# Kernel optimization log

Measured on AMD Instinct MI355X. Metric: run time of the kernel, lower is better.

## Reference

```python
import jax, jax.numpy as jnp
import numpy as np

NUM_HEADS = 8
HEAD_DIM = 64  # hidden_dim // num_heads = 512 // 8
THRESHOLD = 0.5


def setup_inputs() -> dict:
    key = jax.random.key(0)
    ks = jax.random.split(key, 12)
    B, T, D, Hd = 4, 1024, 512, 512
    s = 0.02
    inp = {
        'x': jax.random.normal(ks[0], (B, T, D), dtype=jnp.float32),
        'Wq': jax.random.normal(ks[1], (D, Hd), dtype=jnp.float32) * s,
        'bq': jnp.zeros((Hd,), jnp.float32),
        'Wk': jax.random.normal(ks[2], (D, Hd), dtype=jnp.float32) * s,
        'bk': jnp.zeros((Hd,), jnp.float32),
        'Wv': jax.random.normal(ks[3], (D, Hd), dtype=jnp.float32) * s,
        'bv': jnp.zeros((Hd,), jnp.float32),
        'conv_w': jax.random.normal(ks[4], (NUM_HEADS,), dtype=jnp.float32) * 0.3,
        'conv_b': jnp.zeros((1,), jnp.float32),
        'Wfh': jax.random.normal(ks[5], (Hd, Hd), dtype=jnp.float32) * s,
        'bfh': jnp.zeros((Hd,), jnp.float32),
        'Wfg': jax.random.normal(ks[6], (Hd, Hd), dtype=jnp.float32) * s,
        'bfg': jnp.zeros((Hd,), jnp.float32),
        'Wrh': jax.random.normal(ks[7], (Hd, Hd), dtype=jnp.float32) * s,
        'brh': jnp.zeros((Hd,), jnp.float32),
        'Wrg': jax.random.normal(ks[8], (Hd, Hd), dtype=jnp.float32) * s,
        'brg': jnp.zeros((Hd,), jnp.float32),
    }
    return inp


def reference(x, Wq, bq, Wk, bk, Wv, bv, conv_w, conv_b,
              Wfh, bfh, Wfg, bfg, Wrh, brh, Wrg, brg):
    B, T, D = x.shape
    H, hd = NUM_HEADS, HEAD_DIM
    scale = hd ** -0.5

    q = (x @ Wq + bq).reshape(B, T, H, hd).transpose(0, 2, 1, 3)  # [B,H,T,hd]
    k = (x @ Wk + bk).reshape(B, T, H, hd).transpose(0, 2, 1, 3)
    v = (x @ Wv + bv).reshape(B, T, H, hd).transpose(0, 2, 1, 3)

    scores = jnp.einsum('bhqd,bhkd->bhqk', q, k) * scale        # [B,H,T,T]
    A_t = jax.nn.softmax(scores, axis=-1)

    # cross-head 1x1 conv: weighted sum over heads -> [B,1,T,T]
    R_f = jax.nn.sigmoid(jnp.einsum('bhqk,h->bqk', A_t, conv_w) + conv_b[0])
    R_f = R_f[:, None]                                           # [B,1,T,T]
    M_f = (R_f <= THRESHOLD).astype(A_t.dtype)
    M_r = (1.0 - R_f <= THRESHOLD).astype(A_t.dtype)

    A_f = jax.nn.softmax(A_t * M_f, axis=-1)
    A_r = jax.nn.softmax(A_t * M_r, axis=-1)

    T_f = jnp.einsum('bhqk,bhkd->bhqd', A_f, v).transpose(0, 2, 1, 3).reshape(B, T, H * hd)
    T_r = jnp.einsum('bhqk,bhkd->bhqd', A_r, v).transpose(0, 2, 1, 3).reshape(B, T, H * hd)

    F_f = T_f @ Wfh + bfh
    G_f = jax.nn.sigmoid(T_f @ Wfg + bfg)
    F_r = T_r @ Wrh + brh
    G_r = jax.nn.sigmoid(T_r @ Wrg + brg)

    G_cat = jax.nn.softmax(jnp.stack([G_f, G_r], axis=-1), axis=-1)  # [B,T,Hd,2]
    F_t = F_f * G_cat[..., 0] + F_r * G_cat[..., 1]
    return F_t
```

## Files before the change

### kernel.cpp

```cpp
#include <hip/hip_runtime.h>
#include <hip/hip_bf16.h>
#include <stdint.h>

typedef short bf16x8 __attribute__((ext_vector_type(8)));
typedef float f32x4 __attribute__((ext_vector_type(4)));

__device__ __forceinline__ unsigned short f2bf(float f) {
  union { float f; unsigned int u; } v;
  v.f = f;
  unsigned int u = v.u;
  u = (u + 0x7fffu + ((u >> 16) & 1u)) >> 16;
  return (unsigned short)u;
}

__device__ __forceinline__ unsigned int cvt_pk_bf16(float lo, float hi) {
  unsigned int r;
  asm("v_cvt_pk_bf16_f32 %0, %1, %2" : "=v"(r) : "v"(lo), "v"(hi));
  return r;
}

typedef union { bf16x8 v; unsigned int u[4]; } frag_u;

__device__ __forceinline__ void gload16(const void* g, void* lds) {
  __builtin_amdgcn_global_load_lds(
      (const __attribute__((address_space(1))) unsigned int*)(unsigned long long)g,
      (__attribute__((address_space(3))) unsigned int*)(unsigned long long)(unsigned)(unsigned long long)lds,
      16, 0, 0);
}

__device__ __forceinline__ bf16x8 lds_frag(const unsigned short* t, int row, int ch4q) {
  return *(const bf16x8*)(t + row * 64 + ((ch4q ^ (row & 7)) << 3));
}


__global__ __launch_bounds__(256) void prep_kernel(
    const float* __restrict__ x,
    const float* __restrict__ Wq, const float* __restrict__ Wk, const float* __restrict__ Wv,
    const float* __restrict__ Wfh, const float* __restrict__ Wfg,
    const float* __restrict__ Wrh, const float* __restrict__ Wrg,
    unsigned short* __restrict__ xb, unsigned short* __restrict__ wt) {
  int bid = blockIdx.x;
  int tid = threadIdx.x;
  if (bid < 256) {
    const float4* xi = (const float4*)x;
#pragma unroll
    for (int rep = 0; rep < 8; rep++) {
      int i = bid * 256 + tid + rep * 65536;
      float4 v = xi[i];
      uint2 u;
      u.x = cvt_pk_bf16(v.x, v.y);
      u.y = cvt_pk_bf16(v.z, v.w);
      *(uint2*)&xb[(size_t)i * 4] = u;
    }
  } else {
    __shared__ float tile[64][65];
    int t = bid - 256;
    int mat = t >> 6;
    t &= 63;
    int tr = (t >> 3) * 64, tc = (t & 7) * 64;
    const float* W = (mat == 0) ? Wq : (mat == 1) ? Wk : (mat == 2) ? Wv
                   : (mat == 3) ? Wfh : (mat == 4) ? Wfg : (mat == 5) ? Wrh : Wrg;
    unsigned short* Wt = wt + (size_t)mat * 512 * 512;
    for (int rep = 0; rep < 16; rep++) {
      int idx = rep * 256 + tid;
      int r = idx >> 6, c = idx & 63;
      tile[r][c] = W[(tr + r) * 512 + tc + c];
    }
    __syncthreads();
    for (int rep = 0; rep < 16; rep++) {
      int idx = rep * 256 + tid;
      int r = idx >> 6, c = idx & 63;
      Wt[(tc + r) * 512 + tr + c] = f2bf(tile[c][r]);
    }
  }
}

__global__ __launch_bounds__(256, 2) void qkv_kernel(
    const unsigned short* __restrict__ xb,
    const unsigned short* __restrict__ wtq, const unsigned short* __restrict__ wtk,
    const unsigned short* __restrict__ wtv,
    const float* __restrict__ bq, const float* __restrict__ bk, const float* __restrict__ bv,
    unsigned short* __restrict__ Qfrag, unsigned short* __restrict__ Kfrag,
    unsigned short* __restrict__ Vfrag) {
  __shared__ __attribute__((aligned(16))) unsigned short smem[32768];
  unsigned short* st0 = smem;
  unsigned short* st1 = smem + 4608;
  unsigned short* st2 = smem + 9216;
  const int m0 = blockIdx.y * 64, n0 = blockIdx.x * 64;
  const int tid = threadIdx.x, w = tid >> 6, lane = tid & 63;
  const int c = lane & 15, quad = lane >> 4;
  const int wm = w & 1, wn = w >> 1;
  const int rsel = lane >> 3, csel = lane & 7;
  const int sc = csel ^ rsel;
  const char* Ag  = (const char*)xb  + (size_t)(m0 + w * 16 + rsel) * 1024 + sc * 16;
  const char* Bgq = (const char*)wtq + (size_t)(n0 + w * 16 + rsel) * 1024 + sc * 16;
  const char* Bgk = (const char*)wtk + (size_t)(n0 + w * 16 + rsel) * 1024 + sc * 16;
  const char* Bgv = (const char*)wtv + (size_t)(n0 + w * 16 + rsel) * 1024 + sc * 16;
  const int woff = w * 1024;

  f32x4 acc[3][2][2];
  f32x4 z4 = {0.f, 0.f, 0.f, 0.f};
#pragma unroll
  for (int o = 0; o < 3; o++)
#pragma unroll
    for (int i = 0; i < 2; i++)
#pragma unroll
      for (int j = 0; j < 2; j++) acc[o][i][j] = z4;

  {
    unsigned short* base = smem;
    gload16(Ag, base + woff);              gload16(Ag + 8192, base + woff + 512);
    gload16(Bgq, base + 4096 + woff);      gload16(Bgq + 8192, base + 4096 + woff + 512);
    gload16(Bgk, base + 8192 + woff);      gload16(Bgk + 8192ull + 8192, base + 8192 + woff + 512);
    gload16(Bgv, base + 12288 + woff);     gload16(Bgv + 8192, base + 12288 + woff + 512);
  }
  __syncthreads();

  for (int ks = 0; ks < 8; ks++) {
    unsigned short* cur = smem + (ks & 1) * 16384;
    if (ks < 7) {
      unsigned short* nxt = smem + ((ks + 1) & 1) * 16384;
      const int kb = (ks + 1) * 128;
      gload16(Ag + kb, nxt + woff);          gload16(Ag + kb + 8192, nxt + woff + 512);
      gload16(Bgq + kb, nxt + 4096 + woff);  gload16(Bgq + kb + 8192, nxt + 4096 + woff + 512);
      gload16(Bgk + kb, nxt + 8192 + woff);  gload16(Bgk + kb + 8192, nxt + 8192 + woff + 512);
      gload16(Bgv + kb, nxt + 12288 + woff); gload16(Bgv + kb + 8192, nxt + 12288 + woff + 512);
    }
#pragma unroll
    for (int ch = 0; ch < 2; ch++) {
      const int cq = ch * 4 + quad;
      bf16x8 a0 = lds_frag(cur, wm * 32 + c, cq);
      bf16x8 a1 = lds_frag(cur, wm * 32 + 16 + c, cq);
#pragma unroll
      for (int nt = 0; nt < 2; nt++) {
        const int rb = wn * 32 + nt * 16 + c;
        bf16x8 fq = lds_frag(cur + 4096, rb, cq);
        bf16x8 fk = lds_frag(cur + 8192, rb, cq);
        bf16x8 fv = lds_frag(cur + 12288, rb, cq);
        acc[0][0][nt] = __builtin_amdgcn_mfma_f32_16x16x32_bf16(a0, fq, acc[0][0][nt], 0, 0, 0);
        acc[0][1][nt] = __builtin_amdgcn_mfma_f32_16x16x32_bf16(a1, fq, acc[0][1][nt], 0, 0, 0);
        acc[1][0][nt] = __builtin_amdgcn_mfma_f32_16x16x32_bf16(a0, fk, acc[1][0][nt], 0, 0, 0);
        acc[1][1][nt] = __builtin_amdgcn_mfma_f32_16x16x32_bf16(a1, fk, acc[1][1][nt], 0, 0, 0);
        acc[2][0][nt] = __builtin_amdgcn_mfma_f32_16x16x32_bf16(a0, fv, acc[2][0][nt], 0, 0, 0);
        acc[2][1][nt] = __builtin_amdgcn_mfma_f32_16x16x32_bf16(a1, fv, acc[2][1][nt], 0, 0, 0);
      }
    }
    __syncthreads();
  }

#pragma unroll
  for (int ms = 0; ms < 2; ms++)
#pragma unroll
    for (int nt = 0; nt < 2; nt++) {
      int n_l = wn * 32 + nt * 16 + c;
      int n = n0 + n_l;
      float biasq = bq[n], biask = bk[n], biasv = bv[n];
#pragma unroll
      for (int r = 0; r < 4; r++) {
        int m_l = wm * 32 + ms * 16 + quad * 4 + r;
        st0[m_l * 72 + n_l] = f2bf((acc[0][ms][nt][r] + biasq) * 0.125f);
        st1[m_l * 72 + n_l] = f2bf(acc[1][ms][nt][r] + biask);
        st2[n_l * 72 + m_l] = f2bf(acc[2][ms][nt][r] + biasv);
      }
    }
  __syncthreads();

  {
    const int h = n0 >> 6;
    const int bb = m0 >> 10, t0b = (m0 & 1023) >> 4;
#pragma unroll
    for (int sub = 0; sub < 2; sub++) {
      uint4 vq = *(uint4*)&st0[(w * 16 + c) * 72 + sub * 32 + quad * 8];
      uint4 vk = *(uint4*)&st1[(w * 16 + c) * 72 + sub * 32 + quad * 8];
      size_t base = (size_t)((bb * 64 + t0b + w) * 8192) + h * 1024 + sub * 512 + lane * 8;
      *(uint4*)&Qfrag[base] = vq;
      *(uint4*)&Kfrag[base] = vk;
    }
    const int ktq = t0b + w;
    const int ktp = ktq >> 1, half = ktq & 1;
#pragma unroll
    for (int dm = 0; dm < 4; dm++) {
      uint2 vv = *(uint2*)&st2[(dm * 16 + c) * 72 + w * 16 + quad * 4];
      size_t base = (size_t)(bb * 8 + h) * 65536 + (size_t)(ktp * 4 + dm) * 512
                  + lane * 8 + half * 4;
      *(uint2*)&Vfrag[base] = vv;
    }
  }
}

__global__ __launch_bounds__(512, 2) void attn_kernel(
    const unsigned short* __restrict__ Qfrag, const unsigned short* __restrict__ Kfrag,
    const unsigned short* __restrict__ Vfrag,
    const float* __restrict__ conv_w, const float* __restrict__ conv_b,
    unsigned short* __restrict__ Tfb, unsigned short* __restrict__ Trb) {
  const int b = blockIdx.x, qt = blockIdx.y;
  const int tid = threadIdx.x, w = tid >> 6, lane = tid & 63;
  const int c = lane & 15, quad = lane >> 4;
  __shared__ float zbuf[8][16];
  __shared__ float izbuf[8][16];
  __shared__ __attribute__((aligned(16))) float red[2 * 8 * 4 * 64 * 4];
  __shared__ float zred[2][8][16];

  f32x4 z4 = {0.f, 0.f, 0.f, 0.f};
  const float cb = conv_b[0];
  const size_t qbase = (size_t)((b * 64 + qt) * 8192) + lane * 8;
  const size_t kb0 = (size_t)((b * 64 + w * 8) * 8192) + lane * 8;
  const size_t vb0 = (size_t)(b * 8) * 65536 + lane * 8;

  f32x4 g[8];
#pragma unroll
  for (int j = 0; j < 8; j++) g[j] = {cb, cb, cb, cb};

  for (int h = 0; h < 8; h++) {
    bf16x8 qf0 = *(const bf16x8*)&Qfrag[qbase + h * 1024];
    bf16x8 qf1 = *(const bf16x8*)&Qfrag[qbase + h * 1024 + 512];
    f32x4 p[8];
    float zh = 0.f;
#pragma unroll
    for (int j = 0; j < 8; j++) {
      const size_t kb = kb0 + (size_t)j * 8192 + h * 1024;
      bf16x8 kf0 = *(const bf16x8*)&Kfrag[kb];
      bf16x8 kf1 = *(const bf16x8*)&Kfrag[kb + 512];
      f32x4 s = __builtin_amdgcn_mfma_f32_16x16x32_bf16(kf0, qf0, z4, 0, 0, 0);
      s = __builtin_amdgcn_mfma_f32_16x16x32_bf16(kf1, qf1, s, 0, 0, 0);
      p[j][0] = __expf(s[0]); p[j][1] = __expf(s[1]);
      p[j][2] = __expf(s[2]); p[j][3] = __expf(s[3]);
      zh += (p[j][0] + p[j][1]) + (p[j][2] + p[j][3]);
    }
    zh += __shfl_xor(zh, 16); zh += __shfl_xor(zh, 32);
    __syncthreads();
    if (quad == 0) zbuf[w][c] = zh;
    __syncthreads();
    float Z = ((zbuf[0][c] + zbuf[1][c]) + (zbuf[2][c] + zbuf[3][c]))
            + ((zbuf[4][c] + zbuf[5][c]) + (zbuf[6][c] + zbuf[7][c]));
    const float izq = 1.0f / Z;
    if (w == 0 && quad == 0) izbuf[h][c] = izq;
    const float cwz = conv_w[h] * izq;
#pragma unroll
    for (int j = 0; j < 8; j++) {
      g[j][0] += cwz * p[j][0]; g[j][1] += cwz * p[j][1];
      g[j][2] += cwz * p[j][2]; g[j][3] += cwz * p[j][3];
    }
  }

  unsigned int mmx[4], mmy[4];
#pragma unroll
  for (int t = 0; t < 4; t++) {
    unsigned int p0 = 0, p1 = 0;
#pragma unroll
    for (int r = 0; r < 4; r++) {
      p0 |= ((g[2 * t][r] <= 0.f ? 1u : 0u) | (g[2 * t][r] >= 0.f ? 2u : 0u)) << (8 * r);
      p1 |= ((g[2 * t + 1][r] <= 0.f ? 1u : 0u) | (g[2 * t + 1][r] >= 0.f ? 2u : 0u)) << (8 * r);
    }
    mmx[t] = p0; mmy[t] = p1;
  }
  __syncthreads();

  frag_u ones;
  ones.u[0] = 0x3F803F80u; ones.u[1] = 0x3F803F80u;
  ones.u[2] = 0x3F803F80u; ones.u[3] = 0x3F803F80u;

  const int fr = w >> 2, dmslot = w & 3;
  const size_t tbase = (size_t)(b * 1024 + qt * 16 + c) * 512;
  unsigned short* dstsel = (fr == 0) ? Tfb : Trb;

  for (int h = 0; h < 8; h++) {
    bf16x8 qf0 = *(const bf16x8*)&Qfrag[qbase + h * 1024];
    bf16x8 qf1 = *(const bf16x8*)&Qfrag[qbase + h * 1024 + 512];
    const float iz_h = izbuf[h][c];
    f32x4 accf[4], accr[4];
#pragma unroll
    for (int i = 0; i < 4; i++) { accf[i] = z4; accr[i] = z4; }
    f32x4 zf4 = z4, zr4 = z4;
#pragma unroll
    for (int t = 0; t < 4; t++) {
      const size_t kba = kb0 + (size_t)(2 * t) * 8192 + h * 1024;
      const size_t kbb = kba + 8192;
      bf16x8 ka0 = *(const bf16x8*)&Kfrag[kba];
      bf16x8 ka1 = *(const bf16x8*)&Kfrag[kba + 512];
      bf16x8 kb0f = *(const bf16x8*)&Kfrag[kbb];
      bf16x8 kb1f = *(const bf16x8*)&Kfrag[kbb + 512];
      f32x4 sa = __builtin_amdgcn_mfma_f32_16x16x32_bf16(ka0, qf0, z4, 0, 0, 0);
      sa = __builtin_amdgcn_mfma_f32_16x16x32_bf16(ka1, qf1, sa, 0, 0, 0);
      f32x4 sb = __builtin_amdgcn_mfma_f32_16x16x32_bf16(kb0f, qf0, z4, 0, 0, 0);
      sb = __builtin_amdgcn_mfma_f32_16x16x32_bf16(kb1f, qf1, sb, 0, 0, 0);
      float ea[4], eb[4];
#pragma unroll
      for (int r = 0; r < 4; r++) {
        ea[r] = __expf(__expf(sa[r]) * iz_h);
        eb[r] = __expf(__expf(sb[r]) * iz_h);
      }
      frag_u pF, pR;
      pF.u[0] = cvt_pk_bf16((mmx[t] & 0x1u)       ? ea[0] : 1.f, (mmx[t] & 0x100u)     ? ea[1] : 1.f);
      pF.u[1] = cvt_pk_bf16((mmx[t] & 0x10000u)   ? ea[2] : 1.f, (mmx[t] & 0x1000000u) ? ea[3] : 1.f);
      pF.u[2] = cvt_pk_bf16((mmy[t] & 0x1u)       ? eb[0] : 1.f, (mmy[t] & 0x100u)     ? eb[1] : 1.f);
      pF.u[3] = cvt_pk_bf16((mmy[t] & 0x10000u)   ? eb[2] : 1.f, (mmy[t] & 0x1000000u) ? eb[3] : 1.f);
      pR.u[0] = cvt_pk_bf16((mmx[t] & 0x2u)       ? ea[0] : 1.f, (mmx[t] & 0x200u)     ? ea[1] : 1.f);
      pR.u[1] = cvt_pk_bf16((mmx[t] & 0x20000u)   ? ea[2] : 1.f, (mmx[t] & 0x2000000u) ? ea[3] : 1.f);
      pR.u[2] = cvt_pk_bf16((mmy[t] & 0x2u)       ? eb[0] : 1.f, (mmy[t] & 0x200u)     ? eb[1] : 1.f);
      pR.u[3] = cvt_pk_bf16((mmy[t] & 0x20000u)   ? eb[2] : 1.f, (mmy[t] & 0x2000000u) ? eb[3] : 1.f);
      zf4 = __builtin_amdgcn_mfma_f32_16x16x32_bf16(ones.v, pF.v, zf4, 0, 0, 0);
      zr4 = __builtin_amdgcn_mfma_f32_16x16x32_bf16(ones.v, pR.v, zr4, 0, 0, 0);
      const size_t vbh = vb0 + (size_t)h * 65536 + (size_t)((w * 4 + t) * 4) * 512;
#pragma unroll
      for (int dm = 0; dm < 4; dm++) {
        bf16x8 vf = *(const bf16x8*)&Vfrag[vbh + (size_t)dm * 512];
        accf[dm] = __builtin_amdgcn_mfma_f32_16x16x32_bf16(vf, pF.v, accf[dm], 0, 0, 0);
        accr[dm] = __builtin_amdgcn_mfma_f32_16x16x32_bf16(vf, pR.v, accr[dm], 0, 0, 0);
      }
    }
    __syncthreads();
#pragma unroll
    for (int dm = 0; dm < 4; dm++) {
      *(f32x4*)&red[(((0 * 8 + w) * 4 + dm) * 64 + lane) * 4] = accf[dm];
      *(f32x4*)&red[(((1 * 8 + w) * 4 + dm) * 64 + lane) * 4] = accr[dm];
    }
    if (quad == 0) { zred[0][w][c] = zf4[0]; zred[1][w][c] = zr4[0]; }
    __syncthreads();
    {
      f32x4 o = z4;
#pragma unroll
      for (int w2 = 0; w2 < 8; w2++)
        o += *(const f32x4*)&red[(((fr * 8 + w2) * 4 + dmslot) * 64 + lane) * 4];
      float Zq = 0.f;
#pragma unroll
      for (int w2 = 0; w2 < 8; w2++) Zq += zred[fr][w2][c];
      const float iz = 1.0f / Zq;
      uint2 u;
      u.x = cvt_pk_bf16(o[0] * iz, o[1] * iz);
      u.y = cvt_pk_bf16(o[2] * iz, o[3] * iz);
      *(uint2*)&dstsel[tbase + h * 64 + dmslot * 16 + quad * 4] = u;
    }
  }
}

__global__ __launch_bounds__(256, 4) void final_kernel(
    const unsigned short* __restrict__ Tfb, const unsigned short* __restrict__ Trb,
    const unsigned short* __restrict__ wfh, const unsigned short* __restrict__ wfg,
    const unsigned short* __restrict__ wrh, const unsigned short* __restrict__ wrg,
    const float* __restrict__ bfh, const float* __restrict__ bfg,
    const float* __restrict__ brh, const float* __restrict__ brg,
    float* __restrict__ out) {
  __shared__ unsigned short Atf[32 * 64];
  __shared__ unsigned short Atr[32 * 64];
  __shared__ unsigned short Bfh[64 * 64];
  __shared__ unsigned short Bfg[64 * 64];
  __shared__ unsigned short Brh[64 * 64];
  __shared__ unsigned short Brg[64 * 64];
  const int m0 = blockIdx.y * 32, n0 = blockIdx.x * 64;
  const int tid = threadIdx.x, w = tid >> 6, lane = tid & 63;
  const int c = lane & 15, quad = lane >> 4;
  const int wm = w & 1, wn = w >> 1;
  const int rsel = lane >> 3, csel = lane & 7;
  const int sc = csel ^ rsel;
  const char* Agf = (const char*)Tfb + (size_t)(m0 + w * 8 + rsel) * 1024 + sc * 16;
  const char* Agr = (const char*)Trb + (size_t)(m0 + w * 8 + rsel) * 1024 + sc * 16;
  const char* Bg0 = (const char*)wfh + (size_t)(n0 + w * 16 + rsel) * 1024 + sc * 16;
  const char* Bg1 = (const char*)wfg + (size_t)(n0 + w * 16 + rsel) * 1024 + sc * 16;
  const char* Bg2 = (const char*)wrh + (size_t)(n0 + w * 16 + rsel) * 1024 + sc * 16;
  const char* Bg3 = (const char*)wrg + (size_t)(n0 + w * 16 + rsel) * 1024 + sc * 16;
  unsigned short* lAf = &Atf[w * 512];
  unsigned short* lAr = &Atr[w * 512];
  unsigned short* l0 = &Bfh[w * 1024];
  unsigned short* l1 = &Bfg[w * 1024];
  unsigned short* l2 = &Brh[w * 1024];
  unsigned short* l3 = &Brg[w * 1024];

  f32x4 acc[4][2];
  f32x4 z4 = {0.f, 0.f, 0.f, 0.f};
#pragma unroll
  for (int o = 0; o < 4; o++)
#pragma unroll
    for (int j = 0; j < 2; j++) acc[o][j] = z4;

  for (int ks = 0; ks < 8; ks++) {
    if (ks) __syncthreads();
    const int kb = ks * 128;
    gload16(Agf + kb, lAf);
    gload16(Agr + kb, lAr);
    gload16(Bg0 + kb, l0);   gload16(Bg0 + kb + 8192, l0 + 512);
    gload16(Bg1 + kb, l1);   gload16(Bg1 + kb + 8192, l1 + 512);
    gload16(Bg2 + kb, l2);   gload16(Bg2 + kb + 8192, l2 + 512);
    gload16(Bg3 + kb, l3);   gload16(Bg3 + kb + 8192, l3 + 512);
    __syncthreads();
#pragma unroll
    for (int ch = 0; ch < 2; ch++) {
      const int cq = ch * 4 + quad;
      bf16x8 af = lds_frag(Atf, wm * 16 + c, cq);
      bf16x8 ar = lds_frag(Atr, wm * 16 + c, cq);
#pragma unroll
      for (int nt = 0; nt < 2; nt++) {
        const int rb = wn * 32 + nt * 16 + c;
        bf16x8 f0 = lds_frag(Bfh, rb, cq);
        bf16x8 f1 = lds_frag(Bfg, rb, cq);
        bf16x8 f2 = lds_frag(Brh, rb, cq);
        bf16x8 f3 = lds_frag(Brg, rb, cq);
        acc[0][nt] = __builtin_amdgcn_mfma_f32_16x16x32_bf16(af, f0, acc[0][nt], 0, 0, 0);
        acc[1][nt] = __builtin_amdgcn_mfma_f32_16x16x32_bf16(af, f1, acc[1][nt], 0, 0, 0);
        acc[2][nt] = __builtin_amdgcn_mfma_f32_16x16x32_bf16(ar, f2, acc[2][nt], 0, 0, 0);
        acc[3][nt] = __builtin_amdgcn_mfma_f32_16x16x32_bf16(ar, f3, acc[3][nt], 0, 0, 0);
      }
    }
  }

#pragma unroll
  for (int nt = 0; nt < 2; nt++) {
    int n = n0 + wn * 32 + nt * 16 + c;
    float b0 = bfh[n], b1 = bfg[n], b2 = brh[n], b3 = brg[n];
    int t0 = m0 + wm * 16 + quad * 4;
#pragma unroll
    for (int r = 0; r < 4; r++) {
      int t = t0 + r;
      float Ff = acc[0][nt][r] + b0;
      float Gf = 1.0f / (1.0f + __expf(-(acc[1][nt][r] + b1)));
      float Fr = acc[2][nt][r] + b2;
      float Gr = 1.0f / (1.0f + __expf(-(acc[3][nt][r] + b3)));
      float ef = __expf(Gf), er = __expf(Gr);
      out[(size_t)t * 512 + n] = (Ff * ef + Fr * er) / (ef + er);
    }
  }
}

extern "C" void kernel_launch(void* const* d_in, const int* in_sizes, int n_in,
                              void* d_out, int out_size, void* d_ws, size_t ws_size,
                              hipStream_t stream) {
  const float* x   = (const float*)d_in[0];
  const float* Wq  = (const float*)d_in[1];
  const float* bq  = (const float*)d_in[2];
  const float* Wk  = (const float*)d_in[3];
  const float* bk  = (const float*)d_in[4];
  const float* Wv  = (const float*)d_in[5];
  const float* bv  = (const float*)d_in[6];
  const float* cw  = (const float*)d_in[7];
  const float* cb  = (const float*)d_in[8];
  const float* Wfh = (const float*)d_in[9];
  const float* bfh = (const float*)d_in[10];
  const float* Wfg = (const float*)d_in[11];
  const float* bfg = (const float*)d_in[12];
  const float* Wrh = (const float*)d_in[13];
  const float* brh = (const float*)d_in[14];
  const float* Wrg = (const float*)d_in[15];
  const float* brg = (const float*)d_in[16];

  char* ws = (char*)d_ws;
  const size_t MB = 1024 * 1024;
  unsigned short* xb    = (unsigned short*)(ws + 0 * MB);
  unsigned short* Qfrag = (unsigned short*)(ws + 4 * MB);
  unsigned short* Kfrag = (unsigned short*)(ws + 8 * MB);
  unsigned short* Vfrag = (unsigned short*)(ws + 12 * MB);
  unsigned short* Tfb   = (unsigned short*)(ws + 16 * MB);
  unsigned short* Trb   = (unsigned short*)(ws + 20 * MB);
  unsigned short* wt    = (unsigned short*)(ws + 24 * MB);
  const size_t WSZ = 512 * 512;

  prep_kernel<<<704, 256, 0, stream>>>(x, Wq, Wk, Wv, Wfh, Wfg, Wrh, Wrg, xb, wt);
  qkv_kernel<<<dim3(8, 64), 256, 0, stream>>>(xb, wt + 0 * WSZ, wt + 1 * WSZ, wt + 2 * WSZ,
                                              bq, bk, bv, Qfrag, Kfrag, Vfrag);
  attn_kernel<<<dim3(4, 64), 512, 0, stream>>>(Qfrag, Kfrag, Vfrag, cw, cb, Tfb, Trb);
  final_kernel<<<dim3(8, 128), 256, 0, stream>>>(Tfb, Trb, wt + 3 * WSZ, wt + 4 * WSZ,
                                                 wt + 5 * WSZ, wt + 6 * WSZ,
                                                 bfh, bfg, brh, brg, (float*)d_out);
}
```

Measured before the change: 173.5 us.

## Fix K prologue load offset, pin attn waves, enlarge final GEMM M tile

Fixes the prologue K-weight load in qkv_kernel, which read the wrong second row chunk (offset 16384 instead of 8192) and so fed wrong data into the first k-step. Replaces attn_kernel's launch_bounds min-blocks with an explicit amdgpu_waves_per_eu(2,2) register-budget hint. Doubles final_kernel's M tile from 32 to 64 rows so each weight tile loaded into LDS serves twice as many rows, halving the grid and doubling accumulators per wave. The trade-off is higher register pressure and fewer blocks in the final GEMM.

```diff
diff --git a/kernel.cpp b/kernel.cpp
--- a/kernel.cpp
+++ b/kernel.cpp
@@ -111,7 +111,7 @@
     unsigned short* base = smem;
     gload16(Ag, base + woff);              gload16(Ag + 8192, base + woff + 512);
     gload16(Bgq, base + 4096 + woff);      gload16(Bgq + 8192, base + 4096 + woff + 512);
-    gload16(Bgk, base + 8192 + woff);      gload16(Bgk + 8192ull + 8192, base + 8192 + woff + 512);
+    gload16(Bgk, base + 8192 + woff);      gload16(Bgk + 8192, base + 8192 + woff + 512);
     gload16(Bgv, base + 12288 + woff);     gload16(Bgv + 8192, base + 12288 + woff + 512);
   }
   __syncthreads();
@@ -188,7 +188,9 @@
   }
 }
 
-__global__ __launch_bounds__(512, 2) void attn_kernel(
+__global__ __launch_bounds__(512)
+__attribute__((amdgpu_waves_per_eu(2, 2)))
+void attn_kernel(
     const unsigned short* __restrict__ Qfrag, const unsigned short* __restrict__ Kfrag,
     const unsigned short* __restrict__ Vfrag,
     const float* __restrict__ conv_w, const float* __restrict__ conv_b,
@@ -334,50 +336,52 @@
   }
 }
 
-__global__ __launch_bounds__(256, 4) void final_kernel(
+__global__ __launch_bounds__(256, 2) void final_kernel(
     const unsigned short* __restrict__ Tfb, const unsigned short* __restrict__ Trb,
     const unsigned short* __restrict__ wfh, const unsigned short* __restrict__ wfg,
     const unsigned short* __restrict__ wrh, const unsigned short* __restrict__ wrg,
     const float* __restrict__ bfh, const float* __restrict__ bfg,
     const float* __restrict__ brh, const float* __restrict__ brg,
     float* __restrict__ out) {
-  __shared__ unsigned short Atf[32 * 64];
-  __shared__ unsigned short Atr[32 * 64];
+  __shared__ unsigned short Atf[64 * 64];
+  __shared__ unsigned short Atr[64 * 64];
   __shared__ unsigned short Bfh[64 * 64];
   __shared__ unsigned short Bfg[64 * 64];
   __shared__ unsigned short Brh[64 * 64];
   __shared__ unsigned short Brg[64 * 64];
-  const int m0 = blockIdx.y * 32, n0 = blockIdx.x * 64;
+  const int m0 = blockIdx.y * 64, n0 = blockIdx.x * 64;
   const int tid = threadIdx.x, w = tid >> 6, lane = tid & 63;
   const int c = lane & 15, quad = lane >> 4;
   const int wm = w & 1, wn = w >> 1;
   const int rsel = lane >> 3, csel = lane & 7;
   const int sc = csel ^ rsel;
-  const char* Agf = (const char*)Tfb + (size_t)(m0 + w * 8 + rsel) * 1024 + sc * 16;
-  const char* Agr = (const char*)Trb + (size_t)(m0 + w * 8 + rsel) * 1024 + sc * 16;
+  const char* Agf = (const char*)Tfb + (size_t)(m0 + w * 16 + rsel) * 1024 + sc * 16;
+  const char* Agr = (const char*)Trb + (size_t)(m0 + w * 16 + rsel) * 1024 + sc * 16;
   const char* Bg0 = (const char*)wfh + (size_t)(n0 + w * 16 + rsel) * 1024 + sc * 16;
   const char* Bg1 = (const char*)wfg + (size_t)(n0 + w * 16 + rsel) * 1024 + sc * 16;
   const char* Bg2 = (const char*)wrh + (size_t)(n0 + w * 16 + rsel) * 1024 + sc * 16;
   const char* Bg3 = (const char*)wrg + (size_t)(n0 + w * 16 + rsel) * 1024 + sc * 16;
-  unsigned short* lAf = &Atf[w * 512];
-  unsigned short* lAr = &Atr[w * 512];
+  unsigned short* lAf = &Atf[w * 1024];
+  unsigned short* lAr = &Atr[w * 1024];
   unsigned short* l0 = &Bfh[w * 1024];
   unsigned short* l1 = &Bfg[w * 1024];
   unsigned short* l2 = &Brh[w * 1024];
   unsigned short* l3 = &Brg[w * 1024];
 
-  f32x4 acc[4][2];
+  f32x4 acc[4][2][2];
   f32x4 z4 = {0.f, 0.f, 0.f, 0.f};
 #pragma unroll
   for (int o = 0; o < 4; o++)
 #pragma unroll
-    for (int j = 0; j < 2; j++) acc[o][j] = z4;
+    for (int m = 0; m < 2; m++)
+#pragma unroll
+      for (int j = 0; j < 2; j++) acc[o][m][j] = z4;
 
   for (int ks = 0; ks < 8; ks++) {
     if (ks) __syncthreads();
     const int kb = ks * 128;
-    gload16(Agf + kb, lAf);
-    gload16(Agr + kb, lAr);
+    gload16(Agf + kb, lAf);  gload16(Agf + kb + 8192, lAf + 512);
+    gload16(Agr + kb, lAr);  gload16(Agr + kb + 8192, lAr + 512);
     gload16(Bg0 + kb, l0);   gload16(Bg0 + kb + 8192, l0 + 512);
     gload16(Bg1 + kb, l1);   gload16(Bg1 + kb + 8192, l1 + 512);
     gload16(Bg2 + kb, l2);   gload16(Bg2 + kb + 8192, l2 + 512);
@@ -386,8 +390,10 @@
 #pragma unroll
     for (int ch = 0; ch < 2; ch++) {
       const int cq = ch * 4 + quad;
-      bf16x8 af = lds_frag(Atf, wm * 16 + c, cq);
-      bf16x8 ar = lds_frag(Atr, wm * 16 + c, cq);
+      bf16x8 af0 = lds_frag(Atf, wm * 32 + c, cq);
+      bf16x8 af1 = lds_frag(Atf, wm * 32 + 16 + c, cq);
+      bf16x8 ar0 = lds_frag(Atr, wm * 32 + c, cq);
+      bf16x8 ar1 = lds_frag(Atr, wm * 32 + 16 + c, cq);
 #pragma unroll
       for (int nt = 0; nt < 2; nt++) {
         const int rb = wn * 32 + nt * 16 + c;
@@ -395,10 +401,14 @@
         bf16x8 f1 = lds_frag(Bfg, rb, cq);
         bf16x8 f2 = lds_frag(Brh, rb, cq);
         bf16x8 f3 = lds_frag(Brg, rb, cq);
-        acc[0][nt] = __builtin_amdgcn_mfma_f32_16x16x32_bf16(af, f0, acc[0][nt], 0, 0, 0);
-        acc[1][nt] = __builtin_amdgcn_mfma_f32_16x16x32_bf16(af, f1, acc[1][nt], 0, 0, 0);
-        acc[2][nt] = __builtin_amdgcn_mfma_f32_16x16x32_bf16(ar, f2, acc[2][nt], 0, 0, 0);
-        acc[3][nt] = __builtin_amdgcn_mfma_f32_16x16x32_bf16(ar, f3, acc[3][nt], 0, 0, 0);
+        acc[0][0][nt] = __builtin_amdgcn_mfma_f32_16x16x32_bf16(af0, f0, acc[0][0][nt], 0, 0, 0);
+        acc[0][1][nt] = __builtin_amdgcn_mfma_f32_16x16x32_bf16(af1, f0, acc[0][1][nt], 0, 0, 0);
+        acc[1][0][nt] = __builtin_amdgcn_mfma_f32_16x16x32_bf16(af0, f1, acc[1][0][nt], 0, 0, 0);
+        acc[1][1][nt] = __builtin_amdgcn_mfma_f32_16x16x32_bf16(af1, f1, acc[1][1][nt], 0, 0, 0);
+        acc[2][0][nt] = __builtin_amdgcn_mfma_f32_16x16x32_bf16(ar0, f2, acc[2][0][nt], 0, 0, 0);
+        acc[2][1][nt] = __builtin_amdgcn_mfma_f32_16x16x32_bf16(ar1, f2, acc[2][1][nt], 0, 0, 0);
+        acc[3][0][nt] = __builtin_amdgcn_mfma_f32_16x16x32_bf16(ar0, f3, acc[3][0][nt], 0, 0, 0);
+        acc[3][1][nt] = __builtin_amdgcn_mfma_f32_16x16x32_bf16(ar1, f3, acc[3][1][nt], 0, 0, 0);
       }
     }
   }
@@ -407,16 +417,19 @@
   for (int nt = 0; nt < 2; nt++) {
     int n = n0 + wn * 32 + nt * 16 + c;
     float b0 = bfh[n], b1 = bfg[n], b2 = brh[n], b3 = brg[n];
-    int t0 = m0 + wm * 16 + quad * 4;
-#pragma unroll
-    for (int r = 0; r < 4; r++) {
-      int t = t0 + r;
-      float Ff = acc[0][nt][r] + b0;
-      float Gf = 1.0f / (1.0f + __expf(-(acc[1][nt][r] + b1)));
-      float Fr = acc[2][nt][r] + b2;
-      float Gr = 1.0f / (1.0f + __expf(-(acc[3][nt][r] + b3)));
-      float ef = __expf(Gf), er = __expf(Gr);
-      out[(size_t)t * 512 + n] = (Ff * ef + Fr * er) / (ef + er);
+#pragma unroll
+    for (int m = 0; m < 2; m++) {
+      int t0 = m0 + wm * 32 + m * 16 + quad * 4;
+#pragma unroll
+      for (int r = 0; r < 4; r++) {
+        int t = t0 + r;
+        float Ff = acc[0][m][nt][r] + b0;
+        float Gf = 1.0f / (1.0f + __expf(-(acc[1][m][nt][r] + b1)));
+        float Fr = acc[2][m][nt][r] + b2;
+        float Gr = 1.0f / (1.0f + __expf(-(acc[3][m][nt][r] + b3)));
+        float ef = __expf(Gf), er = __expf(Gr);
+        out[(size_t)t * 512 + n] = (Ff * ef + Fr * er) / (ef + er);
+      }
     }
   }
 }
@@ -457,7 +470,7 @@
   qkv_kernel<<<dim3(8, 64), 256, 0, stream>>>(xb, wt + 0 * WSZ, wt + 1 * WSZ, wt + 2 * WSZ,
                                               bq, bk, bv, Qfrag, Kfrag, Vfrag);
   attn_kernel<<<dim3(4, 64), 512, 0, stream>>>(Qfrag, Kfrag, Vfrag, cw, cb, Tfb, Trb);
-  final_kernel<<<dim3(8, 128), 256, 0, stream>>>(Tfb, Trb, wt + 3 * WSZ, wt + 4 * WSZ,
-                                                 wt + 5 * WSZ, wt + 6 * WSZ,
-                                                 bfh, bfg, brh, brg, (float*)d_out);
-}
+  final_kernel<<<dim3(8, 64), 256, 0, stream>>>(Tfb, Trb, wt + 3 * WSZ, wt + 4 * WSZ,
+                                                wt + 5 * WSZ, wt + 6 * WSZ,
+                                                bfh, bfg, brh, brg, (float*)d_out);
+}
```

Result: slower. 183.9 us (+6.0%).

## Double-buffer LDS tiles in the output GEMM kernel and fix the K-tile offset

Applied to the files above, without the earlier changes.

The final projection/gating kernel moves from a load-sync-compute loop to a two-stage double-buffered LDS pipeline. The next K slice is issued with global_load_lds while MFMAs run on the current slice. The six separate shared arrays become one 2x20480 buffer, which roughly doubles LDS per block, so launch bounds drop from 4 to 2 blocks per SM. Separately, the QKV kernel's prologue had a wrong extra 8192-byte offset on the second K-weight load, and that offset is corrected.

```diff
diff --git a/kernel.cpp b/kernel.cpp
--- a/kernel.cpp
+++ b/kernel.cpp
@@ -111,7 +111,7 @@
     unsigned short* base = smem;
     gload16(Ag, base + woff);              gload16(Ag + 8192, base + woff + 512);
     gload16(Bgq, base + 4096 + woff);      gload16(Bgq + 8192, base + 4096 + woff + 512);
-    gload16(Bgk, base + 8192 + woff);      gload16(Bgk + 8192ull + 8192, base + 8192 + woff + 512);
+    gload16(Bgk, base + 8192 + woff);      gload16(Bgk + 8192, base + 8192 + woff + 512);
     gload16(Bgv, base + 12288 + woff);     gload16(Bgv + 8192, base + 12288 + woff + 512);
   }
   __syncthreads();
@@ -334,19 +334,14 @@
   }
 }
 
-__global__ __launch_bounds__(256, 4) void final_kernel(
+__global__ __launch_bounds__(256, 2) void final_kernel(
     const unsigned short* __restrict__ Tfb, const unsigned short* __restrict__ Trb,
     const unsigned short* __restrict__ wfh, const unsigned short* __restrict__ wfg,
     const unsigned short* __restrict__ wrh, const unsigned short* __restrict__ wrg,
     const float* __restrict__ bfh, const float* __restrict__ bfg,
     const float* __restrict__ brh, const float* __restrict__ brg,
     float* __restrict__ out) {
-  __shared__ unsigned short Atf[32 * 64];
-  __shared__ unsigned short Atr[32 * 64];
-  __shared__ unsigned short Bfh[64 * 64];
-  __shared__ unsigned short Bfg[64 * 64];
-  __shared__ unsigned short Brh[64 * 64];
-  __shared__ unsigned short Brg[64 * 64];
+  __shared__ __attribute__((aligned(16))) unsigned short smem[2][20480];
   const int m0 = blockIdx.y * 32, n0 = blockIdx.x * 64;
   const int tid = threadIdx.x, w = tid >> 6, lane = tid & 63;
   const int c = lane & 15, quad = lane >> 4;
@@ -359,12 +354,8 @@
   const char* Bg1 = (const char*)wfg + (size_t)(n0 + w * 16 + rsel) * 1024 + sc * 16;
   const char* Bg2 = (const char*)wrh + (size_t)(n0 + w * 16 + rsel) * 1024 + sc * 16;
   const char* Bg3 = (const char*)wrg + (size_t)(n0 + w * 16 + rsel) * 1024 + sc * 16;
-  unsigned short* lAf = &Atf[w * 512];
-  unsigned short* lAr = &Atr[w * 512];
-  unsigned short* l0 = &Bfh[w * 1024];
-  unsigned short* l1 = &Bfg[w * 1024];
-  unsigned short* l2 = &Brh[w * 1024];
-  unsigned short* l3 = &Brg[w * 1024];
+  const int aoff = w * 512;
+  const int boff = w * 1024;
 
   f32x4 acc[4][2];
   f32x4 z4 = {0.f, 0.f, 0.f, 0.f};
@@ -373,34 +364,48 @@
 #pragma unroll
     for (int j = 0; j < 2; j++) acc[o][j] = z4;
 
+  {
+    unsigned short* nb = smem[0];
+    gload16(Agf, nb + aoff);
+    gload16(Agr, nb + 2048 + aoff);
+    gload16(Bg0, nb + 4096 + boff);   gload16(Bg0 + 8192, nb + 4096 + boff + 512);
+    gload16(Bg1, nb + 8192 + boff);   gload16(Bg1 + 8192, nb + 8192 + boff + 512);
+    gload16(Bg2, nb + 12288 + boff);  gload16(Bg2 + 8192, nb + 12288 + boff + 512);
+    gload16(Bg3, nb + 16384 + boff);  gload16(Bg3 + 8192, nb + 16384 + boff + 512);
+  }
+  __syncthreads();
+
   for (int ks = 0; ks < 8; ks++) {
-    if (ks) __syncthreads();
-    const int kb = ks * 128;
-    gload16(Agf + kb, lAf);
-    gload16(Agr + kb, lAr);
-    gload16(Bg0 + kb, l0);   gload16(Bg0 + kb + 8192, l0 + 512);
-    gload16(Bg1 + kb, l1);   gload16(Bg1 + kb + 8192, l1 + 512);
-    gload16(Bg2 + kb, l2);   gload16(Bg2 + kb + 8192, l2 + 512);
-    gload16(Bg3 + kb, l3);   gload16(Bg3 + kb + 8192, l3 + 512);
-    __syncthreads();
+    unsigned short* cur = smem[ks & 1];
+    if (ks < 7) {
+      unsigned short* nb = smem[(ks + 1) & 1];
+      const int kb = (ks + 1) * 128;
+      gload16(Agf + kb, nb + aoff);
+      gload16(Agr + kb, nb + 2048 + aoff);
+      gload16(Bg0 + kb, nb + 4096 + boff);   gload16(Bg0 + kb + 8192, nb + 4096 + boff + 512);
+      gload16(Bg1 + kb, nb + 8192 + boff);   gload16(Bg1 + kb + 8192, nb + 8192 + boff + 512);
+      gload16(Bg2 + kb, nb + 12288 + boff);  gload16(Bg2 + kb + 8192, nb + 12288 + boff + 512);
+      gload16(Bg3 + kb, nb + 16384 + boff);  gload16(Bg3 + kb + 8192, nb + 16384 + boff + 512);
+    }
 #pragma unroll
     for (int ch = 0; ch < 2; ch++) {
       const int cq = ch * 4 + quad;
-      bf16x8 af = lds_frag(Atf, wm * 16 + c, cq);
-      bf16x8 ar = lds_frag(Atr, wm * 16 + c, cq);
+      bf16x8 af = lds_frag(cur, wm * 16 + c, cq);
+      bf16x8 ar = lds_frag(cur + 2048, wm * 16 + c, cq);
 #pragma unroll
       for (int nt = 0; nt < 2; nt++) {
         const int rb = wn * 32 + nt * 16 + c;
-        bf16x8 f0 = lds_frag(Bfh, rb, cq);
-        bf16x8 f1 = lds_frag(Bfg, rb, cq);
-        bf16x8 f2 = lds_frag(Brh, rb, cq);
-        bf16x8 f3 = lds_frag(Brg, rb, cq);
+        bf16x8 f0 = lds_frag(cur + 4096, rb, cq);
+        bf16x8 f1 = lds_frag(cur + 8192, rb, cq);
+        bf16x8 f2 = lds_frag(cur + 12288, rb, cq);
+        bf16x8 f3 = lds_frag(cur + 16384, rb, cq);
         acc[0][nt] = __builtin_amdgcn_mfma_f32_16x16x32_bf16(af, f0, acc[0][nt], 0, 0, 0);
         acc[1][nt] = __builtin_amdgcn_mfma_f32_16x16x32_bf16(af, f1, acc[1][nt], 0, 0, 0);
         acc[2][nt] = __builtin_amdgcn_mfma_f32_16x16x32_bf16(ar, f2, acc[2][nt], 0, 0, 0);
         acc[3][nt] = __builtin_amdgcn_mfma_f32_16x16x32_bf16(ar, f3, acc[3][nt], 0, 0, 0);
       }
     }
+    __syncthreads();
   }
 
 #pragma unroll
```

After: 176.7 us. Within noise of the previous version (+1.8%).
